# Optimization experiments

Measured on AMD Instinct MI355X. Metric: run time of the kernel, lower is better.

## Reference

```python
import jax, jax.numpy as jnp
import numpy as np

X1_DIM = 256
X2_DIM = 128
HIDDEN = 256
N = 1024


def _init_linear(key, fan_in, fan_out):
    kw, kb = jax.random.split(key)
    bound = 1.0 / np.sqrt(fan_in)
    W = jax.random.uniform(kw, (fan_in, fan_out), jnp.float32, -bound, bound)
    b = jax.random.uniform(kb, (fan_out,), jnp.float32, -bound, bound)
    return W, b


def setup_inputs() -> dict:
    key = jax.random.key(0)
    k1, k2, k3, k4, k5 = jax.random.split(key, 5)
    x1 = jax.random.normal(k1, (N, X1_DIM), jnp.float32)
    x2 = jax.random.normal(k2, (N, X2_DIM), jnp.float32)
    W1, b1 = _init_linear(k3, X1_DIM, HIDDEN)
    W2, b2 = _init_linear(k4, HIDDEN, HIDDEN)
    W3, b3 = _init_linear(k5, HIDDEN, 2 * X2_DIM)
    return {"x1": x1, "x2": x2, "W1": W1, "b1": b1, "W2": W2, "b2": b2, "W3": W3, "b3": b3}


def reference(x1, x2, W1, b1, W2, b2, W3, b3):
    # gaussian MLP: Linear -> ReLU -> Linear -> ReLU -> Linear -> Tanh
    h = jax.nn.relu(x1 @ W1 + b1)
    h = jax.nn.relu(h @ W2 + b2)
    g = jnp.tanh(h @ W3 + b3)                    # [N, 2*D]
    mu, logvar = jnp.split(g, 2, axis=-1)        # each [N, D]
    inv_var = jnp.exp(-logvar)                   # [N, D]
    # positive term: per-sample conditional log-likelihood
    pos = -0.5 * (mu - x2) ** 2 * inv_var        # [N, D]
    # negative term: pairwise broadcast [N, N, D] then mean over the j axis
    diff2 = (mu[:, None, :] - x2[None, :, :]) ** 2   # [N, N, D]
    neg = -0.5 * diff2.mean(axis=1) * inv_var        # [N, D]
    mi_ub = (pos.sum(axis=-1) - neg.sum(axis=-1)).mean()
    return mi_ub
```

## Files before the change

kernel.cpp:

```cpp
#include <hip/hip_runtime.h>

#define NR 1024
#define ROWS 4
#define NBLK 256
#define NTHR 1024
#define SBLK 32

__global__ __launch_bounds__(256) void stats_kernel(const float* __restrict__ x2,
                                                    float* __restrict__ ws,
                                                    float* __restrict__ out) {
    int tid = threadIdx.x;
    int d = tid & 127;
    int g = tid >> 7;
    int row0 = blockIdx.x * 32 + g;
    float s = 0.f, s2 = 0.f;
#pragma unroll
    for (int i = 0; i < 16; i++) {
        float v = x2[(row0 + 2 * i) * 128 + d];
        s += v;
        s2 += v * v;
    }
    __shared__ float sh[256], sh2[256];
    sh[tid] = s;
    sh2[tid] = s2;
    __syncthreads();
    if (g == 0) {
        ws[blockIdx.x * 256 + d]       = sh[tid] + sh[tid + 128];
        ws[blockIdx.x * 256 + 128 + d] = sh2[tid] + sh2[tid + 128];
    }
    if (blockIdx.x == 0 && tid == 0) out[0] = 0.f;
}

__device__ __forceinline__ void layer(const float* __restrict__ in_lds,
                                      const float* __restrict__ W,
                                      const float* __restrict__ b,
                                      float* __restrict__ out_lds,
                                      float* __restrict__ red,
                                      int g, int q, int act) {
    float acc[8];
#pragma unroll
    for (int e = 0; e < 8; e++) acc[e] = 0.f;
    const float4* in4 = (const float4*)in_lds;
    const float2* Wp = (const float2*)W + g;
    int k0 = q * 32;
#pragma unroll
    for (int j = 0; j < 8; j++) {
        int k = k0 + 4 * j;
        float2 w0 = Wp[(k + 0) * 128];
        float2 w1 = Wp[(k + 1) * 128];
        float2 w2 = Wp[(k + 2) * 128];
        float2 w3 = Wp[(k + 3) * 128];
        float4 xa = in4[0 * 64 + 8 * q + j];
        float4 xb = in4[1 * 64 + 8 * q + j];
        float4 xc = in4[2 * 64 + 8 * q + j];
        float4 xd = in4[3 * 64 + 8 * q + j];
        acc[0] = fmaf(xa.x, w0.x, acc[0]); acc[1] = fmaf(xa.x, w0.y, acc[1]);
        acc[0] = fmaf(xa.y, w1.x, acc[0]); acc[1] = fmaf(xa.y, w1.y, acc[1]);
        acc[0] = fmaf(xa.z, w2.x, acc[0]); acc[1] = fmaf(xa.z, w2.y, acc[1]);
        acc[0] = fmaf(xa.w, w3.x, acc[0]); acc[1] = fmaf(xa.w, w3.y, acc[1]);
        acc[2] = fmaf(xb.x, w0.x, acc[2]); acc[3] = fmaf(xb.x, w0.y, acc[3]);
        acc[2] = fmaf(xb.y, w1.x, acc[2]); acc[3] = fmaf(xb.y, w1.y, acc[3]);
        acc[2] = fmaf(xb.z, w2.x, acc[2]); acc[3] = fmaf(xb.z, w2.y, acc[3]);
        acc[2] = fmaf(xb.w, w3.x, acc[2]); acc[3] = fmaf(xb.w, w3.y, acc[3]);
        acc[4] = fmaf(xc.x, w0.x, acc[4]); acc[5] = fmaf(xc.x, w0.y, acc[5]);
        acc[4] = fmaf(xc.y, w1.x, acc[4]); acc[5] = fmaf(xc.y, w1.y, acc[5]);
        acc[4] = fmaf(xc.z, w2.x, acc[4]); acc[5] = fmaf(xc.z, w2.y, acc[5]);
        acc[4] = fmaf(xc.w, w3.x, acc[4]); acc[5] = fmaf(xc.w, w3.y, acc[5]);
        acc[6] = fmaf(xd.x, w0.x, acc[6]); acc[7] = fmaf(xd.x, w0.y, acc[7]);
        acc[6] = fmaf(xd.y, w1.x, acc[6]); acc[7] = fmaf(xd.y, w1.y, acc[7]);
        acc[6] = fmaf(xd.z, w2.x, acc[6]); acc[7] = fmaf(xd.z, w2.y, acc[7]);
        acc[6] = fmaf(xd.w, w3.x, acc[6]); acc[7] = fmaf(xd.w, w3.y, acc[7]);
    }
#pragma unroll
    for (int e = 0; e < 8; e++) red[q * 1024 + e * 128 + g] = acc[e];
    __syncthreads();
    float s = 0.f;
#pragma unroll
    for (int q2 = 0; q2 < 8; q2++) s += red[q2 * 1024 + q * 128 + g];
    int r = q >> 1;
    int col = 2 * g + (q & 1);
    float v = s + b[col];
    v = act ? tanhf(v) : fmaxf(v, 0.f);
    out_lds[r * 256 + col] = v;
    __syncthreads();
}

__global__ __launch_bounds__(1024, 4) void club_kernel(
    const float* __restrict__ x1, const float* __restrict__ x2,
    const float* __restrict__ W1, const float* __restrict__ b1,
    const float* __restrict__ W2, const float* __restrict__ b2,
    const float* __restrict__ W3, const float* __restrict__ b3,
    const float* __restrict__ part, float* __restrict__ out) {
    __shared__ float bufA[ROWS * 256];
    __shared__ float bufB[ROWS * 256];
    __shared__ float x2s[ROWS * 128];
    __shared__ float stat[256];
    __shared__ float red[8 * 8 * 128];
    __shared__ double dred[16];

    int tid = threadIdx.x;
    int lane = tid & 63, wv = tid >> 6;
    int g = tid & 127;
    int q = tid >> 7;
    int row0 = blockIdx.x * ROWS;

    if (tid < 256) {
        ((float4*)bufA)[tid] = ((const float4*)(x1 + row0 * 256))[tid];
    } else if (tid < 384) {
        ((float4*)x2s)[tid - 256] = ((const float4*)(x2 + row0 * 128))[tid - 256];
    } else if (tid >= 512 && tid < 768) {
        int t = tid - 512;
        float s = 0.f;
#pragma unroll
        for (int p = 0; p < SBLK; p++) s += part[p * 256 + t];
        stat[t] = s * (1.f / 1024.f);
    }
    __syncthreads();

    layer(bufA, W1, b1, bufB, red, g, q, 0);
    layer(bufB, W2, b2, bufA, red, g, q, 0);
    layer(bufA, W3, b3, bufB, red, g, q, 1);

    double p = 0.0;
    if (tid < 512) {
        int d = tid & 127;
        int r = tid >> 7;
        double mu = (double)bufB[r * 256 + d];
        double lv = (double)bufB[r * 256 + 128 + d];
        double xv = (double)x2s[r * 128 + d];
        double mx = (double)stat[d];
        double mxsq = (double)stat[128 + d];
        double iv = exp(-lv);
        p = -0.5 * iv * (xv * xv - mxsq - 2.0 * mu * (xv - mx));
    }
#pragma unroll
    for (int off = 32; off > 0; off >>= 1) p += __shfl_down(p, off, 64);
    if (lane == 0) dred[wv] = p;
    __syncthreads();
    if (tid == 0) {
        double s = 0.0;
#pragma unroll
        for (int i = 0; i < 16; i++) s += dred[i];
        atomicAdd(out, (float)(s * (1.0 / 1024.0)));
    }
}

extern "C" void kernel_launch(void* const* d_in, const int* in_sizes, int n_in,
                              void* d_out, int out_size, void* d_ws, size_t ws_size,
                              hipStream_t stream) {
    const float* x1 = (const float*)d_in[0];
    const float* x2 = (const float*)d_in[1];
    const float* W1 = (const float*)d_in[2];
    const float* b1 = (const float*)d_in[3];
    const float* W2 = (const float*)d_in[4];
    const float* b2 = (const float*)d_in[5];
    const float* W3 = (const float*)d_in[6];
    const float* b3 = (const float*)d_in[7];
    float* out = (float*)d_out;
    float* ws = (float*)d_ws;

    stats_kernel<<<SBLK, 256, 0, stream>>>(x2, ws, out);
    club_kernel<<<NBLK, NTHR, 0, stream>>>(x1, x2, W1, b1, W2, b2, W3, b3, ws, out);
}
```

Measured before the change: 86.02 us.

## Retile MLP layers to float4 weight columns with 16-way K split per wave

Each thread now owns four output columns (float4 weight loads) and each of the 16 waves handles a 16-wide slice of K, instead of two columns and a 32-wide K slice. Partial sums go through a larger LDS reduction buffer (64 KB) and only the first four waves do the final 16-way reduction, bias and activation with vectorized float4 stores. This widens global weight loads and changes the LDS access pattern. The cost is a larger shared-memory footprint, which may limit occupancy, and a longer reduction done by fewer threads.

```diff
diff --git a/kernel.cpp b/kernel.cpp
--- a/kernel.cpp
+++ b/kernel.cpp
@@ -36,52 +36,53 @@
                                       const float* __restrict__ b,
                                       float* __restrict__ out_lds,
                                       float* __restrict__ red,
-                                      int g, int q, int act) {
-    float acc[8];
+                                      int l, int q, int act) {
+    float4 acc[4];
 #pragma unroll
-    for (int e = 0; e < 8; e++) acc[e] = 0.f;
+    for (int r = 0; r < 4; r++) acc[r] = make_float4(0.f, 0.f, 0.f, 0.f);
     const float4* in4 = (const float4*)in_lds;
-    const float2* Wp = (const float2*)W + g;
-    int k0 = q * 32;
+    const float4* Wp = (const float4*)W + l;
+    int k0 = q * 16;
 #pragma unroll
-    for (int j = 0; j < 8; j++) {
-        int k = k0 + 4 * j;
-        float2 w0 = Wp[(k + 0) * 128];
-        float2 w1 = Wp[(k + 1) * 128];
-        float2 w2 = Wp[(k + 2) * 128];
-        float2 w3 = Wp[(k + 3) * 128];
-        float4 xa = in4[0 * 64 + 8 * q + j];
-        float4 xb = in4[1 * 64 + 8 * q + j];
-        float4 xc = in4[2 * 64 + 8 * q + j];
-        float4 xd = in4[3 * 64 + 8 * q + j];
-        acc[0] = fmaf(xa.x, w0.x, acc[0]); acc[1] = fmaf(xa.x, w0.y, acc[1]);
-        acc[0] = fmaf(xa.y, w1.x, acc[0]); acc[1] = fmaf(xa.y, w1.y, acc[1]);
-        acc[0] = fmaf(xa.z, w2.x, acc[0]); acc[1] = fmaf(xa.z, w2.y, acc[1]);
-        acc[0] = fmaf(xa.w, w3.x, acc[0]); acc[1] = fmaf(xa.w, w3.y, acc[1]);
-        acc[2] = fmaf(xb.x, w0.x, acc[2]); acc[3] = fmaf(xb.x, w0.y, acc[3]);
-        acc[2] = fmaf(xb.y, w1.x, acc[2]); acc[3] = fmaf(xb.y, w1.y, acc[3]);
-        acc[2] = fmaf(xb.z, w2.x, acc[2]); acc[3] = fmaf(xb.z, w2.y, acc[3]);
-        acc[2] = fmaf(xb.w, w3.x, acc[2]); acc[3] = fmaf(xb.w, w3.y, acc[3]);
-        acc[4] = fmaf(xc.x, w0.x, acc[4]); acc[5] = fmaf(xc.x, w0.y, acc[5]);
-        acc[4] = fmaf(xc.y, w1.x, acc[4]); acc[5] = fmaf(xc.y, w1.y, acc[5]);
-        acc[4] = fmaf(xc.z, w2.x, acc[4]); acc[5] = fmaf(xc.z, w2.y, acc[5]);
-        acc[4] = fmaf(xc.w, w3.x, acc[4]); acc[5] = fmaf(xc.w, w3.y, acc[5]);
-        acc[6] = fmaf(xd.x, w0.x, acc[6]); acc[7] = fmaf(xd.x, w0.y, acc[7]);
-        acc[6] = fmaf(xd.y, w1.x, acc[6]); acc[7] = fmaf(xd.y, w1.y, acc[7]);
-        acc[6] = fmaf(xd.z, w2.x, acc[6]); acc[7] = fmaf(xd.z, w2.y, acc[7]);
-        acc[6] = fmaf(xd.w, w3.x, acc[6]); acc[7] = fmaf(xd.w, w3.y, acc[7]);
+    for (int j = 0; j < 4; j++) {
+        float4 w0 = Wp[(k0 + 4 * j + 0) * 64];
+        float4 w1 = Wp[(k0 + 4 * j + 1) * 64];
+        float4 w2 = Wp[(k0 + 4 * j + 2) * 64];
+        float4 w3 = Wp[(k0 + 4 * j + 3) * 64];
+#pragma unroll
+        for (int r = 0; r < 4; r++) {
+            float4 xr = in4[r * 64 + 4 * q + j];
+            acc[r].x = fmaf(xr.x, w0.x, acc[r].x); acc[r].y = fmaf(xr.x, w0.y, acc[r].y);
+            acc[r].z = fmaf(xr.x, w0.z, acc[r].z); acc[r].w = fmaf(xr.x, w0.w, acc[r].w);
+            acc[r].x = fmaf(xr.y, w1.x, acc[r].x); acc[r].y = fmaf(xr.y, w1.y, acc[r].y);
+            acc[r].z = fmaf(xr.y, w1.z, acc[r].z); acc[r].w = fmaf(xr.y, w1.w, acc[r].w);
+            acc[r].x = fmaf(xr.z, w2.x, acc[r].x); acc[r].y = fmaf(xr.z, w2.y, acc[r].y);
+            acc[r].z = fmaf(xr.z, w2.z, acc[r].z); acc[r].w = fmaf(xr.z, w2.w, acc[r].w);
+            acc[r].x = fmaf(xr.w, w3.x, acc[r].x); acc[r].y = fmaf(xr.w, w3.y, acc[r].y);
+            acc[r].z = fmaf(xr.w, w3.z, acc[r].z); acc[r].w = fmaf(xr.w, w3.w, acc[r].w);
+        }
     }
+    float4* red4 = (float4*)red;
 #pragma unroll
-    for (int e = 0; e < 8; e++) red[q * 1024 + e * 128 + g] = acc[e];
+    for (int r = 0; r < 4; r++) red4[q * 256 + r * 64 + l] = acc[r];
     __syncthreads();
-    float s = 0.f;
+    if (q < 4) {
+        float4 s = make_float4(0.f, 0.f, 0.f, 0.f);
 #pragma unroll
-    for (int q2 = 0; q2 < 8; q2++) s += red[q2 * 1024 + q * 128 + g];
-    int r = q >> 1;
-    int col = 2 * g + (q & 1);
-    float v = s + b[col];
-    v = act ? tanhf(v) : fmaxf(v, 0.f);
-    out_lds[r * 256 + col] = v;
+        for (int q2 = 0; q2 < 16; q2++) {
+            float4 v = red4[q2 * 256 + q * 64 + l];
+            s.x += v.x; s.y += v.y; s.z += v.z; s.w += v.w;
+        }
+        float4 bb = ((const float4*)b)[l];
+        s.x += bb.x; s.y += bb.y; s.z += bb.z; s.w += bb.w;
+        if (act) {
+            s.x = tanhf(s.x); s.y = tanhf(s.y); s.z = tanhf(s.z); s.w = tanhf(s.w);
+        } else {
+            s.x = fmaxf(s.x, 0.f); s.y = fmaxf(s.y, 0.f);
+            s.z = fmaxf(s.z, 0.f); s.w = fmaxf(s.w, 0.f);
+        }
+        ((float4*)out_lds)[q * 64 + l] = s;
+    }
     __syncthreads();
 }
 
@@ -95,13 +96,11 @@
     __shared__ float bufB[ROWS * 256];
     __shared__ float x2s[ROWS * 128];
     __shared__ float stat[256];
-    __shared__ float red[8 * 8 * 128];
+    __shared__ float red[16 * 1024];
     __shared__ double dred[16];
 
     int tid = threadIdx.x;
     int lane = tid & 63, wv = tid >> 6;
-    int g = tid & 127;
-    int q = tid >> 7;
     int row0 = blockIdx.x * ROWS;
 
     if (tid < 256) {
@@ -117,9 +116,9 @@
     }
     __syncthreads();
 
-    layer(bufA, W1, b1, bufB, red, g, q, 0);
-    layer(bufB, W2, b2, bufA, red, g, q, 0);
-    layer(bufA, W3, b3, bufB, red, g, q, 1);
+    layer(bufA, W1, b1, bufB, red, lane, wv, 0);
+    layer(bufB, W2, b2, bufA, red, lane, wv, 0);
+    layer(bufA, W3, b3, bufB, red, lane, wv, 1);
 
     double p = 0.0;
     if (tid < 512) {
```

New measurement: 82.96 us. -3.6%, faster.
